# Performance work log

Measured on AMD Instinct MI355X. Metric: run time of the kernel, lower is better.

## Reference

```python
import jax, jax.numpy as jnp
import numpy as np


def setup_inputs() -> dict:
    key = jax.random.key(0)
    ks = jax.random.split(key, 6)
    B, C, H, W, Q = 16, 64, 64, 64, 8192
    HID = 256
    K = C * 9  # 576, unfolded channel count and srnet out_dim (co_mat=1)
    feat = jax.random.normal(ks[0], (B, C, H, W), jnp.float32)
    coord = jax.random.uniform(ks[1], (B, Q, 2), jnp.float32) * 2.0 - 1.0  # normalized [-1,1]
    cell = jnp.ones((B, Q, 2), jnp.float32) * (2.0 / 128.0)  # HR cell size for 128-px grid
    w1 = jax.random.normal(ks[2], (3, HID), jnp.float32) / np.sqrt(3.0)
    b1 = jnp.zeros((HID,), jnp.float32)
    w2 = jax.random.normal(ks[3], (HID, HID), jnp.float32) / np.sqrt(float(HID))
    b2 = jnp.zeros((HID,), jnp.float32)
    w3 = jax.random.normal(ks[4], (HID, K), jnp.float32) / np.sqrt(float(HID))
    b3 = jnp.zeros((K,), jnp.float32)
    return {"feat": feat, "coord": coord, "cell": cell,
            "w1": w1, "b1": b1, "w2": w2, "b2": b2, "w3": w3, "b3": b3}


def reference(feat, coord, cell, w1, b1, w2, b2, w3, b3):
    B, C, H, W = feat.shape
    Q = coord.shape[1]
    K = C * 9
    co_mat = 1
    # F.unfold(feat, 3, padding=1).view(B, C*9, H, W): channel-major, kernel pos minor
    padded = jnp.pad(feat, ((0, 0), (0, 0), (1, 1), (1, 1)))
    patches = jnp.stack([padded[:, :, i:i + H, j:j + W]
                         for i in range(3) for j in range(3)], axis=2)  # [B,C,9,H,W]
    featu = patches.reshape(B, K, H * W)
    # shift query coords by half a cell
    coord_ = coord - cell / 2.0
    coord_q = jnp.clip(coord_ + 1e-6, -1.0 + 1e-6, 1.0 - 1e-6)
    # nearest grid_sample, align_corners=False: idx = round(((c+1)*S - 1)/2)
    # coord[...,0] indexes H (grid y after flip), coord[...,1] indexes W (grid x)
    iy = jnp.clip(jnp.round(((coord_q[..., 0] + 1.0) * H - 1.0) / 2.0), 0, H - 1).astype(jnp.int32)
    ix = jnp.clip(jnp.round(((coord_q[..., 1] + 1.0) * W - 1.0) / 2.0), 0, W - 1).astype(jnp.int32)
    lin = iy * W + ix  # [B,Q]
    q_feat = jnp.take_along_axis(featu, lin[:, None, :], axis=2).transpose(0, 2, 1)  # [B,Q,K]
    # q_coord: make_coord value minus half-pixel shift at the nearest index = 2i/S - 1 (exact)
    qy = 2.0 * iy.astype(jnp.float32) / H - 1.0
    qx = 2.0 * ix.astype(jnp.float32) / W - 1.0
    rel_y = (coord_[..., 0] - qy) * (H / 2.0)
    rel_x = (coord_[..., 1] - qx) * (W / 2.0)
    r_rev = cell[..., 0] * (H / 2.0)
    inp = jnp.stack([rel_y, rel_x, r_rev], axis=-1)  # [B,Q,3]
    # srnet MLP: per-query filter of shape [K, co_mat]
    h = jax.nn.relu(inp @ w1 + b1)
    h = jax.nn.relu(h @ w2 + b2)
    wmat = (h @ w3 + b3).reshape(B, Q, K, co_mat)
    # bmm combine: [1,K] @ [K,co_mat] per query
    pred = jnp.einsum('bqk,bqkc->bqc', q_feat, wmat)  # [B,Q,1]
    return pred
```

## Files before the change

kernel.cpp:

```cpp
#include <hip/hip_runtime.h>
#include <hip/hip_bf16.h>

#define BB 16
#define CC 64
#define HH 64
#define WW 64
#define QQ 8192
#define HID 256
#define KK 576
#define HT 66
#define FROW 264

typedef short short8 __attribute__((ext_vector_type(8)));
typedef short sv4    __attribute__((ext_vector_type(4)));
typedef float f32x4  __attribute__((ext_vector_type(4)));

__device__ __forceinline__ short f2bf(float f) {
    union { float f; unsigned u; } v; v.f = f;
    unsigned r = v.u + 0x7fffu + ((v.u >> 16) & 1u);
    return (short)(r >> 16);
}
__device__ __forceinline__ float bf2f(short s) {
    union { unsigned u; float f; } v; v.u = ((unsigned)(unsigned short)s) << 16;
    return v.f;
}
__device__ __forceinline__ void barrier_lds() {
    asm volatile("s_waitcnt lgkmcnt(0)" ::: "memory");
    __builtin_amdgcn_s_barrier();
    asm volatile("" ::: "memory");
}

__global__ __launch_bounds__(256) void prep_transpose_k(const float* __restrict__ feat,
                                                        const float* __restrict__ w2,
                                                        const float* __restrict__ w3,
                                                        const float* __restrict__ b3,
                                                        short* __restrict__ featT,
                                                        short* __restrict__ w3cB,
                                                        short* __restrict__ w2cB) {
    __shared__ float ftile[64][65];
    const int t = threadIdx.x;
    const int gidx = blockIdx.x * 256 + t;

    if (gidx < 156672) {
        int kchunk = gidx / 2176;
        int rem = gidx - kchunk * 2176;
        int n = rem >> 3, j = rem & 7;
        int kglob = kchunk * 8 + j;
        int pos = kglob >> 6, c = kglob & 63;
        float v = 0.f;
        if (n < 256)      v = w3[n * KK + c * 9 + pos];
        else if (n == 256) v = b3[c * 9 + pos];
        w3cB[gidx] = f2bf(v);
    }
    if (gidx < 65536) {
        int kchunk = gidx >> 11;
        int rem = gidx & 2047;
        int n = rem >> 3, j = rem & 7;
        int k = kchunk * 8 + j;
        w2cB[gidx] = f2bf(w2[k * 256 + n]);
    }

    const int b = blockIdx.x / HT;
    const int yy = blockIdx.x - b * HT;
    short* out_row = featT + ((b * HT + yy) * HT) * 64;

    if (yy == 0 || yy == HT - 1) {
        for (int idx = t; idx < HT * 64; idx += 256) out_row[idx] = 0;
        return;
    }
    const int y = yy - 1;
    const float* src = feat + ((b * CC) * HH + y) * WW;
#pragma unroll
    for (int i = 0; i < 16; ++i) {
        int idx = i * 256 + t;
        int c = idx >> 6, x = idx & 63;
        ftile[c][x] = src[c * (HH * WW) + x];
    }
    if (t < 64) out_row[t] = 0;
    else if (t < 128) out_row[(HT - 1) * 64 + (t - 64)] = 0;
    __syncthreads();
#pragma unroll
    for (int i = 0; i < 16; ++i) {
        int idx = i * 256 + t;
        int x = idx >> 6, c = idx & 63;
        out_row[(x + 1) * 64 + c] = f2bf(ftile[c][x]);
    }
}

#define SSTR 72
__global__ __launch_bounds__(256, 2) void conv_k(const short* __restrict__ featT,
                                                 const short* __restrict__ w3cB,
                                                 short* __restrict__ F) {
    __shared__ short slab[3 * HT * SSTR];
    const int t = threadIdx.x;
    const int wave = t >> 6, lane = t & 63, quad = lane >> 4, ln16 = lane & 15;
    const int b = blockIdx.x >> 6, y = blockIdx.x & 63;

    f32x4 acc[4][5];
#pragma unroll
    for (int a = 0; a < 4; ++a)
#pragma unroll
        for (int i = 0; i < 5; ++i) acc[a][i] = (f32x4){0.f, 0.f, 0.f, 0.f};

    short8 bbuf[3][5];
    const short* bbase = w3cB + (quad * 272 + ln16) * 8;
    auto loadB = [&](int st, int slot) {
#pragma unroll
        for (int i = 0; i < 5; ++i) {
            int sub = (i < 4) ? (wave + 4 * i) : 16;
            bbuf[slot][i] = *(const short8*)(bbase + st * 8704 + sub * 128);
        }
    };

    loadB(0, 0);
    loadB(1, 1);

    const short* slabsrc = featT + b * (HT * HT * 64) + y * (HT * 64);
#pragma unroll
    for (int it = 0; it < 7; ++it) {
        int i = it * 256 + t;
        if (i < 1584) {
            short8 v = *(const short8*)(slabsrc + i * 8);
            int row = i >> 3, cs = (i & 7) * 8;
            *(short8*)(&slab[row * SSTR + cs]) = v;
        }
    }
    barrier_lds();

#pragma unroll
    for (int st = 0; st < 18; ++st) {
        if (st < 16) loadB(st + 2, (st + 2) % 3);
        const int pos = st >> 1, ks = st & 1;
        const int di = pos / 3, dj = pos - di * 3;
        short8 af[4];
#pragma unroll
        for (int ms = 0; ms < 4; ++ms)
            af[ms] = *(const short8*)(&slab[(di * HT + ms * 16 + ln16 + dj) * SSTR + ks * 32 + quad * 8]);
#pragma unroll
        for (int i = 0; i < 5; ++i)
#pragma unroll
            for (int ms = 0; ms < 4; ++ms)
                acc[ms][i] = __builtin_amdgcn_mfma_f32_16x16x32_bf16(af[ms], bbuf[st % 3][i], acc[ms][i], 0, 0, 0);
    }

#pragma unroll
    for (int h = 0; h < 2; ++h) {
        if (h) barrier_lds();
#pragma unroll
        for (int i = 0; i < 5; ++i) {
            int sub = (i < 4) ? (wave + 4 * i) : 16;
            int n = sub * 16 + ln16;
            bool store = (i < 4) || (wave == 0 && n < FROW);
            if (store) {
#pragma unroll
                for (int ms2 = 0; ms2 < 2; ++ms2) {
                    int ms = h * 2 + ms2;
#pragma unroll
                    for (int r = 0; r < 4; ++r) {
                        int xl = ms2 * 16 + quad * 4 + r;
                        slab[xl * FROW + n] = f2bf(acc[ms][i][r]);
                    }
                }
            }
        }
        barrier_lds();
        short8* dst = (short8*)(F + ((long)(b * 64 + y) * 64 + h * 32) * FROW);
        const short8* src8 = (const short8*)slab;
#pragma unroll
        for (int it = 0; it < 5; ++it) {
            int idx = it * 256 + t;
            if (idx < (32 * FROW) / 8) dst[idx] = src8[idx];
        }
    }
}

#define HSTR 264
__global__ __launch_bounds__(256, 3) void mlp_k(const float* __restrict__ coord,
                                                const float* __restrict__ cell,
                                                const float* __restrict__ w1,
                                                const float* __restrict__ b1,
                                                const float* __restrict__ b2v,
                                                const short* __restrict__ w2cB,
                                                const short* __restrict__ F,
                                                float* __restrict__ out) {
    __shared__ short Hh[64 * HSTR];
    __shared__ float red_s[64][4];

    const int t = threadIdx.x;
    const int wave = t >> 6, lane = t & 63, quad = lane >> 4, ln16 = lane & 15;
    const int qbase = blockIdx.x * 64;
    const int b = qbase >> 13;

    short8 wbuf[3][4];
    const short* w2base = w2cB + (quad * 256 + wave * 64 + ln16) * 8;
    auto loadW = [&](int s, int slot) {
#pragma unroll
        for (int i = 0; i < 4; ++i)
            wbuf[slot][i] = *(const short8*)(w2base + s * 8192 + i * 128);
    };

    const int g = qbase + lane;
    const float2 cc = *(const float2*)(coord + g * 2);
    const float2 ce = *(const float2*)(cell + g * 2);

    loadW(0, 0);
    loadW(1, 1);

    const float coy = cc.x - ce.x * 0.5f, cox = cc.y - ce.y * 0.5f;
    const float cqy = fminf(fmaxf(coy + 1e-6f, -0.999999f), 0.999999f);
    const float cqx = fminf(fmaxf(cox + 1e-6f, -0.999999f), 0.999999f);
    int iy = (int)rintf(((cqy + 1.0f) * 64.0f - 1.0f) * 0.5f); iy = min(max(iy, 0), 63);
    int ix = (int)rintf(((cqx + 1.0f) * 64.0f - 1.0f) * 0.5f); ix = min(max(ix, 0), 63);
    const int lin = iy * 64 + ix;
    const float in0 = (coy - ((float)iy * (1.0f / 32.0f) - 1.0f)) * 32.0f;
    const float in1 = (cox - ((float)ix * (1.0f / 32.0f) - 1.0f)) * 32.0f;
    const float in2 = ce.x * 32.0f;

    int linm[4];
#pragma unroll
    for (int ms = 0; ms < 4; ++ms) linm[ms] = __shfl(lin, ms * 16 + ln16, 64);

    short8 hv[8];
    const int k0w = wave * 64;
#pragma unroll
    for (int c8 = 0; c8 < 8; ++c8) {
        const int k0 = k0w + c8 * 8;
        f32x4 wa0 = *(const f32x4*)(w1 + k0),       wa1 = *(const f32x4*)(w1 + k0 + 4);
        f32x4 wb0 = *(const f32x4*)(w1 + 256 + k0), wb1 = *(const f32x4*)(w1 + 256 + k0 + 4);
        f32x4 wc0 = *(const f32x4*)(w1 + 512 + k0), wc1 = *(const f32x4*)(w1 + 512 + k0 + 4);
        f32x4 bb0 = *(const f32x4*)(b1 + k0),       bb1 = *(const f32x4*)(b1 + k0 + 4);
#pragma unroll
        for (int jj = 0; jj < 4; ++jj) {
            float v0 = fmaf(in0, wa0[jj], fmaf(in1, wb0[jj], fmaf(in2, wc0[jj], bb0[jj])));
            float v1 = fmaf(in0, wa1[jj], fmaf(in1, wb1[jj], fmaf(in2, wc1[jj], bb1[jj])));
            hv[c8][jj]     = f2bf(fmaxf(v0, 0.f));
            hv[c8][jj + 4] = f2bf(fmaxf(v1, 0.f));
        }
    }
#pragma unroll
    for (int c8 = 0; c8 < 8; ++c8)
        *(short8*)(&Hh[lane * HSTR + wave * 64 + c8 * 8]) = hv[c8];
    barrier_lds();

    const short* Fb = F + (long)b * 4096 * FROW;
    sv4 fv[4][4];
    short fbs = 0;
    f32x4 b2q[4];
    f32x4 acc2[4][4];
#pragma unroll
    for (int i = 0; i < 4; ++i)
#pragma unroll
        for (int ms = 0; ms < 4; ++ms) acc2[i][ms] = (f32x4){0.f, 0.f, 0.f, 0.f};

#pragma unroll
    for (int s = 0; s < 8; ++s) {
        if (s < 6) loadW(s + 2, (s + 2) % 3);
        short8 hf[4];
#pragma unroll
        for (int ms = 0; ms < 4; ++ms)
            hf[ms] = *(const short8*)(&Hh[(ms * 16 + ln16) * HSTR + s * 32 + quad * 8]);
        if (s == 6) {
#pragma unroll
            for (int ms = 0; ms < 4; ++ms) {
                const short* Fr = Fb + (long)linm[ms] * FROW + wave * 64 + quad * 4;
#pragma unroll
                for (int i = 0; i < 4; ++i) fv[ms][i] = *(const sv4*)(Fr + i * 16);
            }
            fbs = Fb[(long)lin * FROW + 256];
        }
        if (s == 7) {
#pragma unroll
            for (int i = 0; i < 4; ++i)
                b2q[i] = *(const f32x4*)(b2v + wave * 64 + i * 16 + quad * 4);
        }
#pragma unroll
        for (int i = 0; i < 4; ++i)
#pragma unroll
            for (int ms = 0; ms < 4; ++ms)
                acc2[i][ms] = __builtin_amdgcn_mfma_f32_16x16x32_bf16(wbuf[s % 3][i], hf[ms], acc2[i][ms], 0, 0, 0);
    }

    const float fbv = bf2f(fbs);
    float part[4] = {0.f, 0.f, 0.f, 0.f};
#pragma unroll
    for (int i = 0; i < 4; ++i)
#pragma unroll
        for (int ms = 0; ms < 4; ++ms)
#pragma unroll
            for (int r = 0; r < 4; ++r)
                part[ms] = fmaf(fmaxf(acc2[i][ms][r] + b2q[i][r], 0.f), bf2f(fv[ms][i][r]), part[ms]);
#pragma unroll
    for (int ms = 0; ms < 4; ++ms) {
        part[ms] += __shfl_xor(part[ms], 16, 64);
        part[ms] += __shfl_xor(part[ms], 32, 64);
    }
    if (quad == 0) {
#pragma unroll
        for (int ms = 0; ms < 4; ++ms) red_s[ms * 16 + ln16][wave] = part[ms];
    }
    barrier_lds();
    if (t < 64)
        out[qbase + t] = red_s[t][0] + red_s[t][1] + red_s[t][2] + red_s[t][3] + fbv;
}

extern "C" void kernel_launch(void* const* d_in, const int* in_sizes, int n_in,
                              void* d_out, int out_size, void* d_ws, size_t ws_size,
                              hipStream_t stream) {
    const float* feat  = (const float*)d_in[0];
    const float* coord = (const float*)d_in[1];
    const float* cell  = (const float*)d_in[2];
    const float* w1    = (const float*)d_in[3];
    const float* b1    = (const float*)d_in[4];
    const float* w2    = (const float*)d_in[5];
    const float* b2    = (const float*)d_in[6];
    const float* w3    = (const float*)d_in[7];
    const float* b3    = (const float*)d_in[8];
    float* out = (float*)d_out;

    char* ws = (char*)d_ws;
    short* w3cB  = (short*)(ws);
    short* w2cB  = (short*)(ws + 313344);
    short* featT = (short*)(ws + 444416);
    short* F     = (short*)(ws + 9365504);
    (void)ws_size; (void)in_sizes; (void)n_in; (void)out_size;

    prep_transpose_k<<<BB * HT, 256, 0, stream>>>(feat, w2, w3, b3, featT, w3cB, w2cB);
    conv_k<<<BB * HH, 256, 0, stream>>>(featT, w3cB, F);
    mlp_k<<<(BB * QQ) / 64, 256, 0, stream>>>(coord, cell, w1, b1, b2, w2cB, F, out);
}
```

Baseline: 152.2 us.

## Prefetch gathered feature rows into LDS via async global_load_lds early in mlp_k

New measurement: 152.7 us. No clear change (+0.3%).

```diff
diff --git a/kernel.cpp b/kernel.cpp
--- a/kernel.cpp
+++ b/kernel.cpp
@@ -28,6 +28,11 @@
     asm volatile("s_waitcnt lgkmcnt(0)" ::: "memory");
     __builtin_amdgcn_s_barrier();
     asm volatile("" ::: "memory");
+}
+__device__ __forceinline__ void glld16(const short* g, short* l) {
+    __builtin_amdgcn_global_load_lds(
+        (const __attribute__((address_space(1))) void*)g,
+        (__attribute__((address_space(3))) void*)l, 16, 0, 0);
 }
 
 __global__ __launch_bounds__(256) void prep_transpose_k(const float* __restrict__ feat,
@@ -174,8 +179,7 @@
     }
 }
 
-#define HSTR 264
-__global__ __launch_bounds__(256, 3) void mlp_k(const float* __restrict__ coord,
+__global__ __launch_bounds__(256, 2) void mlp_k(const float* __restrict__ coord,
                                                 const float* __restrict__ cell,
                                                 const float* __restrict__ w1,
                                                 const float* __restrict__ b1,
@@ -183,8 +187,8 @@
                                                 const short* __restrict__ w2cB,
                                                 const short* __restrict__ F,
                                                 float* __restrict__ out) {
-    __shared__ short Hh[64 * HSTR];
-    __shared__ float red_s[64][4];
+    __shared__ short HhF[16384];
+    __shared__ short FLds[16384];
 
     const int t = threadIdx.x;
     const int wave = t >> 6, lane = t & 63, quad = lane >> 4, ln16 = lane & 15;
@@ -216,9 +220,16 @@
     const float in1 = (cox - ((float)ix * (1.0f / 32.0f) - 1.0f)) * 32.0f;
     const float in2 = ce.x * 32.0f;
 
-    int linm[4];
-#pragma unroll
-    for (int ms = 0; ms < 4; ++ms) linm[ms] = __shfl(lin, ms * 16 + ln16, 64);
+    const short* Fb = F + (long)b * 4096 * FROW;
+    const short fbs = Fb[(long)lin * FROW + 256];
+
+#pragma unroll
+    for (int j = 0; j < 8; ++j) {
+        const int r = 2 * (wave * 8 + j) + (lane >> 5);
+        const int linr = __shfl(lin, r, 64);
+        const int colb = ((lane & 31) * 16) ^ ((r & 7) << 4);
+        glld16(Fb + (long)linr * FROW + (colb >> 1), &FLds[(wave * 8 + j) * 512]);
+    }
 
     short8 hv[8];
     const int k0w = wave * 64;
@@ -239,12 +250,9 @@
     }
 #pragma unroll
     for (int c8 = 0; c8 < 8; ++c8)
-        *(short8*)(&Hh[lane * HSTR + wave * 64 + c8 * 8]) = hv[c8];
+        *(short8*)(&HhF[((2 * wave + (c8 >> 2)) * 4 + (c8 & 3)) * 512 + lane * 8]) = hv[c8];
     barrier_lds();
 
-    const short* Fb = F + (long)b * 4096 * FROW;
-    sv4 fv[4][4];
-    short fbs = 0;
     f32x4 b2q[4];
     f32x4 acc2[4][4];
 #pragma unroll
@@ -258,16 +266,7 @@
         short8 hf[4];
 #pragma unroll
         for (int ms = 0; ms < 4; ++ms)
-            hf[ms] = *(const short8*)(&Hh[(ms * 16 + ln16) * HSTR + s * 32 + quad * 8]);
-        if (s == 6) {
-#pragma unroll
-            for (int ms = 0; ms < 4; ++ms) {
-                const short* Fr = Fb + (long)linm[ms] * FROW + wave * 64 + quad * 4;
-#pragma unroll
-                for (int i = 0; i < 4; ++i) fv[ms][i] = *(const sv4*)(Fr + i * 16);
-            }
-            fbs = Fb[(long)lin * FROW + 256];
-        }
+            hf[ms] = *(const short8*)(&HhF[(s * 4 + quad) * 512 + (ms * 16 + ln16) * 8]);
         if (s == 7) {
 #pragma unroll
             for (int i = 0; i < 4; ++i)
@@ -280,27 +279,38 @@
                 acc2[i][ms] = __builtin_amdgcn_mfma_f32_16x16x32_bf16(wbuf[s % 3][i], hf[ms], acc2[i][ms], 0, 0, 0);
     }
 
+    __syncthreads();
+
     const float fbv = bf2f(fbs);
     float part[4] = {0.f, 0.f, 0.f, 0.f};
-#pragma unroll
-    for (int i = 0; i < 4; ++i)
-#pragma unroll
-        for (int ms = 0; ms < 4; ++ms)
-#pragma unroll
-            for (int r = 0; r < 4; ++r)
-                part[ms] = fmaf(fmaxf(acc2[i][ms][r] + b2q[i][r], 0.f), bf2f(fv[ms][i][r]), part[ms]);
+    const char* FLb = (const char*)FLds;
+#pragma unroll
+    for (int ms = 0; ms < 4; ++ms) {
+        const int r = ms * 16 + ln16;
+        const int xr = (r & 7) << 4;
+        const int rb = r * 512;
+#pragma unroll
+        for (int i = 0; i < 4; ++i) {
+            sv4 fvv = *(const sv4*)(FLb + rb + ((wave * 128 + i * 32 + quad * 8) ^ xr));
+#pragma unroll
+            for (int r4 = 0; r4 < 4; ++r4)
+                part[ms] = fmaf(fmaxf(acc2[i][ms][r4] + b2q[i][r4], 0.f), bf2f(fvv[r4]), part[ms]);
+        }
+    }
 #pragma unroll
     for (int ms = 0; ms < 4; ++ms) {
         part[ms] += __shfl_xor(part[ms], 16, 64);
         part[ms] += __shfl_xor(part[ms], 32, 64);
     }
+    barrier_lds();
+    float* red = (float*)FLds;
     if (quad == 0) {
 #pragma unroll
-        for (int ms = 0; ms < 4; ++ms) red_s[ms * 16 + ln16][wave] = part[ms];
+        for (int ms = 0; ms < 4; ++ms) red[(ms * 16 + ln16) * 4 + wave] = part[ms];
     }
     barrier_lds();
     if (t < 64)
-        out[qbase + t] = red_s[t][0] + red_s[t][1] + red_s[t][2] + red_s[t][3] + fbv;
+        out[qbase + t] = red[t * 4 + 0] + red[t * 4 + 1] + red[t * 4 + 2] + red[t * 4 + 3] + fbv;
 }
 
 extern "C" void kernel_launch(void* const* d_in, const int* in_sizes, int n_in,
```

## Map images to XCDs, split conv/MLP into two halves, retile MLP H layout

Applied to the files above, without the earlier changes.

Measured after the change: 184.8 us. 21.4% more time.

```diff
diff --git a/kernel.cpp b/kernel.cpp
--- a/kernel.cpp
+++ b/kernel.cpp
@@ -29,6 +29,7 @@
     __builtin_amdgcn_s_barrier();
     asm volatile("" ::: "memory");
 }
+
 
 __global__ __launch_bounds__(256) void prep_transpose_k(const float* __restrict__ feat,
                                                         const float* __restrict__ w2,
@@ -60,8 +61,10 @@
         w2cB[gidx] = f2bf(w2[k * 256 + n]);
     }
 
-    const int b = blockIdx.x / HT;
-    const int yy = blockIdx.x - b * HT;
+    const int x = blockIdx.x & 7;
+    const int i = blockIdx.x >> 3;
+    const int b  = (i < 66) ? x : (x + 8);
+    const int yy = (i < 66) ? i : (i - 66);
     short* out_row = featT + ((b * HT + yy) * HT) * 64;
 
     if (yy == 0 || yy == HT - 1) {
@@ -71,30 +74,33 @@
     const int y = yy - 1;
     const float* src = feat + ((b * CC) * HH + y) * WW;
 #pragma unroll
-    for (int i = 0; i < 16; ++i) {
-        int idx = i * 256 + t;
-        int c = idx >> 6, x = idx & 63;
-        ftile[c][x] = src[c * (HH * WW) + x];
+    for (int i2 = 0; i2 < 16; ++i2) {
+        int idx = i2 * 256 + t;
+        int c = idx >> 6, xx = idx & 63;
+        ftile[c][xx] = src[c * (HH * WW) + xx];
     }
     if (t < 64) out_row[t] = 0;
     else if (t < 128) out_row[(HT - 1) * 64 + (t - 64)] = 0;
     __syncthreads();
 #pragma unroll
-    for (int i = 0; i < 16; ++i) {
-        int idx = i * 256 + t;
-        int x = idx >> 6, c = idx & 63;
-        out_row[(x + 1) * 64 + c] = f2bf(ftile[c][x]);
+    for (int i2 = 0; i2 < 16; ++i2) {
+        int idx = i2 * 256 + t;
+        int xx = idx >> 6, c = idx & 63;
+        out_row[(xx + 1) * 64 + c] = f2bf(ftile[c][xx]);
     }
 }
 
 #define SSTR 72
 __global__ __launch_bounds__(256, 2) void conv_k(const short* __restrict__ featT,
                                                  const short* __restrict__ w3cB,
-                                                 short* __restrict__ F) {
+                                                 short* __restrict__ F,
+                                                 int img_off) {
     __shared__ short slab[3 * HT * SSTR];
     const int t = threadIdx.x;
     const int wave = t >> 6, lane = t & 63, quad = lane >> 4, ln16 = lane & 15;
-    const int b = blockIdx.x >> 6, y = blockIdx.x & 63;
+    const int xcd = blockIdx.x & 7;
+    const int b = xcd + img_off;
+    const int y = blockIdx.x >> 3;
 
     f32x4 acc[4][5];
 #pragma unroll
@@ -174,7 +180,6 @@
     }
 }
 
-#define HSTR 264
 __global__ __launch_bounds__(256, 3) void mlp_k(const float* __restrict__ coord,
                                                 const float* __restrict__ cell,
                                                 const float* __restrict__ w1,
@@ -182,125 +187,136 @@
                                                 const float* __restrict__ b2v,
                                                 const short* __restrict__ w2cB,
                                                 const short* __restrict__ F,
-                                                float* __restrict__ out) {
-    __shared__ short Hh[64 * HSTR];
+                                                float* __restrict__ out,
+                                                int img_off) {
+    __shared__ short HhF[16384];
     __shared__ float red_s[64][4];
 
     const int t = threadIdx.x;
     const int wave = t >> 6, lane = t & 63, quad = lane >> 4, ln16 = lane & 15;
-    const int qbase = blockIdx.x * 64;
-    const int b = qbase >> 13;
+    const int xcd = blockIdx.x & 7;
+    const int slot = blockIdx.x >> 3;
+    const int b = xcd + img_off;
+    const int qbase0 = b * QQ + slot * 128;
+
+    const float2 cc0 = *(const float2*)(coord + (qbase0 + lane) * 2);
+    const float2 ce0 = *(const float2*)(cell + (qbase0 + lane) * 2);
+    const float2 cc1 = *(const float2*)(coord + (qbase0 + 64 + lane) * 2);
+    const float2 ce1 = *(const float2*)(cell + (qbase0 + 64 + lane) * 2);
+
+    const short* w2base = w2cB + (quad * 256 + wave * 64 + ln16) * 8;
+    const short* Fb = F + (long)b * 4096 * FROW;
 
     short8 wbuf[3][4];
-    const short* w2base = w2cB + (quad * 256 + wave * 64 + ln16) * 8;
-    auto loadW = [&](int s, int slot) {
+    auto loadW = [&](int ss, int sl) {
 #pragma unroll
         for (int i = 0; i < 4; ++i)
-            wbuf[slot][i] = *(const short8*)(w2base + s * 8192 + i * 128);
+            wbuf[sl][i] = *(const short8*)(w2base + ss * 8192 + i * 128);
     };
 
-    const int g = qbase + lane;
-    const float2 cc = *(const float2*)(coord + g * 2);
-    const float2 ce = *(const float2*)(cell + g * 2);
-
-    loadW(0, 0);
-    loadW(1, 1);
-
-    const float coy = cc.x - ce.x * 0.5f, cox = cc.y - ce.y * 0.5f;
-    const float cqy = fminf(fmaxf(coy + 1e-6f, -0.999999f), 0.999999f);
-    const float cqx = fminf(fmaxf(cox + 1e-6f, -0.999999f), 0.999999f);
-    int iy = (int)rintf(((cqy + 1.0f) * 64.0f - 1.0f) * 0.5f); iy = min(max(iy, 0), 63);
-    int ix = (int)rintf(((cqx + 1.0f) * 64.0f - 1.0f) * 0.5f); ix = min(max(ix, 0), 63);
-    const int lin = iy * 64 + ix;
-    const float in0 = (coy - ((float)iy * (1.0f / 32.0f) - 1.0f)) * 32.0f;
-    const float in1 = (cox - ((float)ix * (1.0f / 32.0f) - 1.0f)) * 32.0f;
-    const float in2 = ce.x * 32.0f;
-
-    int linm[4];
-#pragma unroll
-    for (int ms = 0; ms < 4; ++ms) linm[ms] = __shfl(lin, ms * 16 + ln16, 64);
-
-    short8 hv[8];
-    const int k0w = wave * 64;
-#pragma unroll
-    for (int c8 = 0; c8 < 8; ++c8) {
-        const int k0 = k0w + c8 * 8;
-        f32x4 wa0 = *(const f32x4*)(w1 + k0),       wa1 = *(const f32x4*)(w1 + k0 + 4);
-        f32x4 wb0 = *(const f32x4*)(w1 + 256 + k0), wb1 = *(const f32x4*)(w1 + 256 + k0 + 4);
-        f32x4 wc0 = *(const f32x4*)(w1 + 512 + k0), wc1 = *(const f32x4*)(w1 + 512 + k0 + 4);
-        f32x4 bb0 = *(const f32x4*)(b1 + k0),       bb1 = *(const f32x4*)(b1 + k0 + 4);
-#pragma unroll
-        for (int jj = 0; jj < 4; ++jj) {
-            float v0 = fmaf(in0, wa0[jj], fmaf(in1, wb0[jj], fmaf(in2, wc0[jj], bb0[jj])));
-            float v1 = fmaf(in0, wa1[jj], fmaf(in1, wb1[jj], fmaf(in2, wc1[jj], bb1[jj])));
-            hv[c8][jj]     = f2bf(fmaxf(v0, 0.f));
-            hv[c8][jj + 4] = f2bf(fmaxf(v1, 0.f));
-        }
-    }
-#pragma unroll
-    for (int c8 = 0; c8 < 8; ++c8)
-        *(short8*)(&Hh[lane * HSTR + wave * 64 + c8 * 8]) = hv[c8];
-    barrier_lds();
-
-    const short* Fb = F + (long)b * 4096 * FROW;
-    sv4 fv[4][4];
-    short fbs = 0;
-    f32x4 b2q[4];
-    f32x4 acc2[4][4];
-#pragma unroll
-    for (int i = 0; i < 4; ++i)
-#pragma unroll
-        for (int ms = 0; ms < 4; ++ms) acc2[i][ms] = (f32x4){0.f, 0.f, 0.f, 0.f};
-
-#pragma unroll
-    for (int s = 0; s < 8; ++s) {
-        if (s < 6) loadW(s + 2, (s + 2) % 3);
-        short8 hf[4];
-#pragma unroll
-        for (int ms = 0; ms < 4; ++ms)
-            hf[ms] = *(const short8*)(&Hh[(ms * 16 + ln16) * HSTR + s * 32 + quad * 8]);
-        if (s == 6) {
-#pragma unroll
-            for (int ms = 0; ms < 4; ++ms) {
-                const short* Fr = Fb + (long)linm[ms] * FROW + wave * 64 + quad * 4;
-#pragma unroll
-                for (int i = 0; i < 4; ++i) fv[ms][i] = *(const sv4*)(Fr + i * 16);
+#pragma unroll
+    for (int it2 = 0; it2 < 2; ++it2) {
+        const int qbase = qbase0 + it2 * 64;
+        const float2 cc = it2 ? cc1 : cc0;
+        const float2 ce = it2 ? ce1 : ce0;
+
+        loadW(0, 0);
+        loadW(1, 1);
+
+        const float coy = cc.x - ce.x * 0.5f, cox = cc.y - ce.y * 0.5f;
+        const float cqy = fminf(fmaxf(coy + 1e-6f, -0.999999f), 0.999999f);
+        const float cqx = fminf(fmaxf(cox + 1e-6f, -0.999999f), 0.999999f);
+        int iy = (int)rintf(((cqy + 1.0f) * 64.0f - 1.0f) * 0.5f); iy = min(max(iy, 0), 63);
+        int ix = (int)rintf(((cqx + 1.0f) * 64.0f - 1.0f) * 0.5f); ix = min(max(ix, 0), 63);
+        const int lin = iy * 64 + ix;
+        const float in0 = (coy - ((float)iy * (1.0f / 32.0f) - 1.0f)) * 32.0f;
+        const float in1 = (cox - ((float)ix * (1.0f / 32.0f) - 1.0f)) * 32.0f;
+        const float in2 = ce.x * 32.0f;
+
+        int linm[4];
+#pragma unroll
+        for (int ms = 0; ms < 4; ++ms) linm[ms] = __shfl(lin, ms * 16 + ln16, 64);
+
+        sv4 fv[4][4];
+#pragma unroll
+        for (int ms = 0; ms < 4; ++ms) {
+            const short* Fr = Fb + (long)linm[ms] * FROW + wave * 64 + quad * 4;
+#pragma unroll
+            for (int i = 0; i < 4; ++i) fv[ms][i] = *(const sv4*)(Fr + i * 16);
+        }
+        const short fbs = Fb[(long)lin * FROW + 256];
+
+        short8 hv[8];
+        const int k0w = wave * 64;
+#pragma unroll
+        for (int c8 = 0; c8 < 8; ++c8) {
+            const int k0 = k0w + c8 * 8;
+            f32x4 wa0 = *(const f32x4*)(w1 + k0),       wa1 = *(const f32x4*)(w1 + k0 + 4);
+            f32x4 wb0 = *(const f32x4*)(w1 + 256 + k0), wb1 = *(const f32x4*)(w1 + 256 + k0 + 4);
+            f32x4 wc0 = *(const f32x4*)(w1 + 512 + k0), wc1 = *(const f32x4*)(w1 + 512 + k0 + 4);
+            f32x4 bb0 = *(const f32x4*)(b1 + k0),       bb1 = *(const f32x4*)(b1 + k0 + 4);
+#pragma unroll
+            for (int jj = 0; jj < 4; ++jj) {
+                float v0 = fmaf(in0, wa0[jj], fmaf(in1, wb0[jj], fmaf(in2, wc0[jj], bb0[jj])));
+                float v1 = fmaf(in0, wa1[jj], fmaf(in1, wb1[jj], fmaf(in2, wc1[jj], bb1[jj])));
+                hv[c8][jj]     = f2bf(fmaxf(v0, 0.f));
+                hv[c8][jj + 4] = f2bf(fmaxf(v1, 0.f));
             }
-            fbs = Fb[(long)lin * FROW + 256];
-        }
-        if (s == 7) {
+        }
+#pragma unroll
+        for (int c8 = 0; c8 < 8; ++c8)
+            *(short8*)(&HhF[((2 * wave + (c8 >> 2)) * 4 + (c8 & 3)) * 512 + lane * 8]) = hv[c8];
+        barrier_lds();
+
+        f32x4 b2q[4];
+        f32x4 acc2[4][4];
+#pragma unroll
+        for (int i = 0; i < 4; ++i)
+#pragma unroll
+            for (int ms = 0; ms < 4; ++ms) acc2[i][ms] = (f32x4){0.f, 0.f, 0.f, 0.f};
+
+#pragma unroll
+        for (int ss = 0; ss < 8; ++ss) {
+            if (ss < 6) loadW(ss + 2, (ss + 2) % 3);
+            short8 hf[4];
+#pragma unroll
+            for (int ms = 0; ms < 4; ++ms)
+                hf[ms] = *(const short8*)(&HhF[(ss * 4 + quad) * 512 + (ms * 16 + ln16) * 8]);
+            if (ss == 7) {
+#pragma unroll
+                for (int i = 0; i < 4; ++i)
+                    b2q[i] = *(const f32x4*)(b2v + wave * 64 + i * 16 + quad * 4);
+            }
 #pragma unroll
             for (int i = 0; i < 4; ++i)
-                b2q[i] = *(const f32x4*)(b2v + wave * 64 + i * 16 + quad * 4);
-        }
+#pragma unroll
+                for (int ms = 0; ms < 4; ++ms)
+                    acc2[i][ms] = __builtin_amdgcn_mfma_f32_16x16x32_bf16(wbuf[ss % 3][i], hf[ms], acc2[i][ms], 0, 0, 0);
+        }
+
+        const float fbv = bf2f(fbs);
+        float part[4] = {0.f, 0.f, 0.f, 0.f};
 #pragma unroll
         for (int i = 0; i < 4; ++i)
 #pragma unroll
             for (int ms = 0; ms < 4; ++ms)
-                acc2[i][ms] = __builtin_amdgcn_mfma_f32_16x16x32_bf16(wbuf[s % 3][i], hf[ms], acc2[i][ms], 0, 0, 0);
-    }
-
-    const float fbv = bf2f(fbs);
-    float part[4] = {0.f, 0.f, 0.f, 0.f};
-#pragma unroll
-    for (int i = 0; i < 4; ++i)
-#pragma unroll
-        for (int ms = 0; ms < 4; ++ms)
-#pragma unroll
-            for (int r = 0; r < 4; ++r)
-                part[ms] = fmaf(fmaxf(acc2[i][ms][r] + b2q[i][r], 0.f), bf2f(fv[ms][i][r]), part[ms]);
-#pragma unroll
-    for (int ms = 0; ms < 4; ++ms) {
-        part[ms] += __shfl_xor(part[ms], 16, 64);
-        part[ms] += __shfl_xor(part[ms], 32, 64);
-    }
-    if (quad == 0) {
-#pragma unroll
-        for (int ms = 0; ms < 4; ++ms) red_s[ms * 16 + ln16][wave] = part[ms];
-    }
-    barrier_lds();
-    if (t < 64)
-        out[qbase + t] = red_s[t][0] + red_s[t][1] + red_s[t][2] + red_s[t][3] + fbv;
+#pragma unroll
+                for (int r = 0; r < 4; ++r)
+                    part[ms] = fmaf(fmaxf(acc2[i][ms][r] + b2q[i][r], 0.f), bf2f(fv[ms][i][r]), part[ms]);
+#pragma unroll
+        for (int ms = 0; ms < 4; ++ms) {
+            part[ms] += __shfl_xor(part[ms], 16, 64);
+            part[ms] += __shfl_xor(part[ms], 32, 64);
+        }
+        barrier_lds();
+        if (quad == 0) {
+#pragma unroll
+            for (int ms = 0; ms < 4; ++ms) red_s[ms * 16 + ln16][wave] = part[ms];
+        }
+        barrier_lds();
+        if (t < 64)
+            out[qbase + t] = red_s[t][0] + red_s[t][1] + red_s[t][2] + red_s[t][3] + fbv;
+    }
 }
 
 extern "C" void kernel_launch(void* const* d_in, const int* in_sizes, int n_in,
@@ -325,6 +341,8 @@
     (void)ws_size; (void)in_sizes; (void)n_in; (void)out_size;
 
     prep_transpose_k<<<BB * HT, 256, 0, stream>>>(feat, w2, w3, b3, featT, w3cB, w2cB);
-    conv_k<<<BB * HH, 256, 0, stream>>>(featT, w3cB, F);
-    mlp_k<<<(BB * QQ) / 64, 256, 0, stream>>>(coord, cell, w1, b1, b2, w2cB, F, out);
-}
+    conv_k<<<512, 256, 0, stream>>>(featT, w3cB, F, 8);
+    mlp_k<<<512, 256, 0, stream>>>(coord, cell, w1, b1, b2, w2cB, F, out, 8);
+    conv_k<<<512, 256, 0, stream>>>(featT, w3cB, F, 0);
+    mlp_k<<<512, 256, 0, stream>>>(coord, cell, w1, b1, b2, w2cB, F, out, 0);
+}
```
